# Kernel tuning notes

Measured on AMD Instinct MI355X. Metric: run time of the kernel, lower is better.

Reference implementation:

```python
import jax, jax.numpy as jnp
import numpy as np

N = 50000
E = 800000
D_IN, D_HID, D_OUT = 256, 512, 256
LN_EPS = 1e-5


def setup_inputs() -> dict:
    key = jax.random.key(0)
    ks = jax.random.split(key, 8)
    return {
        "v": jax.random.normal(ks[0], (N, D_IN), dtype=jnp.float32),
        "edge_weight": jax.random.uniform(ks[1], (E,), dtype=jnp.float32),
        "epsilon": jnp.zeros((1, 1), dtype=jnp.float32),
        "w1": jax.random.normal(ks[2], (D_HID, D_IN), dtype=jnp.float32) * (1.0 / np.sqrt(D_IN)),
        "b1": jnp.zeros((D_HID,), dtype=jnp.float32),
        "g1": jnp.ones((D_HID,), dtype=jnp.float32),
        "beta1": jnp.zeros((D_HID,), dtype=jnp.float32),
        "w2": jax.random.normal(ks[3], (D_OUT, D_HID), dtype=jnp.float32) * (1.0 / np.sqrt(D_HID)),
        "b2": jnp.zeros((D_OUT,), dtype=jnp.float32),
        "g2": jnp.ones((D_OUT,), dtype=jnp.float32),
        "beta2": jnp.zeros((D_OUT,), dtype=jnp.float32),
        "src": jax.random.randint(ks[4], (E,), 0, N, dtype=jnp.int32),
        "dst": jax.random.randint(ks[5], (E,), 0, N, dtype=jnp.int32),
    }


def _layer_norm(x, g, b):
    mu = jnp.mean(x, axis=-1, keepdims=True)
    var = jnp.mean(jnp.square(x - mu), axis=-1, keepdims=True)
    return (x - mu) * jax.lax.rsqrt(var + LN_EPS) * g + b


def reference(v, edge_weight, epsilon, w1, b1, g1, beta1, w2, b2, g2, beta2, src, dst):
    # sparse adjacency aggregation: agg[dst] += w * v[src]   (torch.sparse.mm(a, v))
    msgs = v[src] * edge_weight[:, None]            # [E, D_IN]
    agg = jax.ops.segment_sum(msgs, dst, num_segments=v.shape[0])  # [N, D_IN]
    h = agg + epsilon * v                            # epsilon residual
    # MLP: Linear -> LayerNorm -> ReLU  (x2)
    h = jax.nn.relu(_layer_norm(h @ w1.T + b1, g1, beta1))
    h = jax.nn.relu(_layer_norm(h @ w2.T + b2, g2, beta2))
    return h
```

## Files before the change

kernel.cpp:

```cpp
#include <hip/hip_runtime.h>

#define D_IN 256
#define D_HID 512
#define D_OUT 256
#define LN_EPS 1e-5f
#define SCAN_B 512

typedef __attribute__((ext_vector_type(8))) short bf16x8;
typedef __attribute__((ext_vector_type(4))) float f32x4;

__device__ __forceinline__ ushort f2bf(float x) {
    union { float f; unsigned u; } c; c.f = x;
    unsigned r = c.u + 0x7FFFu + ((c.u >> 16) & 1u);
    return (ushort)(r >> 16);
}
__device__ __forceinline__ float bf2f(unsigned b) {
    union { unsigned u; float f; } c; c.u = b << 16;
    return c.f;
}

__global__ void prep_kernel(const float* __restrict__ v, const float* __restrict__ w1,
                            const float* __restrict__ w2, ushort* __restrict__ vb,
                            ushort* __restrict__ w1b, ushort* __restrict__ w2b,
                            int* __restrict__ cnt, int n4v, int nzero,
                            int bv, int bw) {
    int b = blockIdx.x, t = threadIdx.x;
    if (b < bv) {
        int i = b * 256 + t;
        if (i < n4v) {
            float4 x = ((const float4*)v)[i];
            ((ushort4*)vb)[i] = make_ushort4(f2bf(x.x), f2bf(x.y), f2bf(x.z), f2bf(x.w));
        }
    } else if (b < bv + bw) {
        int j = (b - bv) * 256 + t;
        if (j < 32768) {
            float4 x = ((const float4*)w1)[j];
            ((ushort4*)w1b)[j] = make_ushort4(f2bf(x.x), f2bf(x.y), f2bf(x.z), f2bf(x.w));
        } else {
            int k = j - 32768;
            float4 x = ((const float4*)w2)[k];
            ((ushort4*)w2b)[k] = make_ushort4(f2bf(x.x), f2bf(x.y), f2bf(x.z), f2bf(x.w));
        }
    } else {
        int i = (b - bv - bw) * 256 + t;
        if (i < nzero) cnt[i] = 0;
    }
}

__global__ void hist_kernel(const int* __restrict__ dst, int* __restrict__ cnt, int E) {
    int e = blockIdx.x * 256 + threadIdx.x;
    if (e < E) atomicAdd(&cnt[dst[e]], 1);
}

__global__ __launch_bounds__(SCAN_B) void scan1_kernel(const int* __restrict__ cnt,
                                                       int* __restrict__ offs,
                                                       int* __restrict__ bsum, int n) {
    __shared__ int s[SCAN_B];
    int i = blockIdx.x * SCAN_B + threadIdx.x;
    int x = (i < n) ? cnt[i] : 0;
    s[threadIdx.x] = x;
    __syncthreads();
    for (int o = 1; o < SCAN_B; o <<= 1) {
        int t = (threadIdx.x >= (unsigned)o) ? s[threadIdx.x - o] : 0;
        __syncthreads();
        s[threadIdx.x] += t;
        __syncthreads();
    }
    if (i < n) offs[i] = s[threadIdx.x] - x;
    if (threadIdx.x == SCAN_B - 1) bsum[blockIdx.x] = s[threadIdx.x];
}

__global__ __launch_bounds__(SCAN_B) void scan3_kernel(int* __restrict__ offs,
                                                       int* __restrict__ cursor,
                                                       const int* __restrict__ bsum,
                                                       int n, int E, int nb) {
    __shared__ int s[SCAN_B];
    int t = threadIdx.x;
    s[t] = (t < nb && t < (int)blockIdx.x) ? bsum[t] : 0;
    __syncthreads();
    for (int o = SCAN_B / 2; o > 0; o >>= 1) {
        if (t < o) s[t] += s[t + o];
        __syncthreads();
    }
    int base = s[0];
    int i = blockIdx.x * SCAN_B + t;
    if (i < n) {
        int v0 = offs[i] + base;
        offs[i] = v0;
        cursor[i] = v0;
    }
    if (i == 0) offs[n] = E;
}

__global__ void fill_kernel(const int* __restrict__ src, const int* __restrict__ dst,
                            const float* __restrict__ ew, int* __restrict__ cursor,
                            int2* __restrict__ perm, int E) {
    int e = blockIdx.x * 256 + threadIdx.x;
    if (e >= E) return;
    int p = atomicAdd(&cursor[dst[e]], 1);
    perm[p] = make_int2(src[e], __float_as_int(ew[e]));
}

__global__ __launch_bounds__(256) void aggregate_kernel(
    const ushort* __restrict__ vb, const float* __restrict__ eps_p,
    const int* __restrict__ offs, const int2* __restrict__ perm,
    ushort* __restrict__ aggb, int N) {
    int node = blockIdx.x * 4 + (threadIdx.x >> 6);
    if (node >= N) return;
    int lane = threadIdx.x & 63;
    int beg = offs[node], end = offs[node + 1];
    float a0 = 0.f, a1 = 0.f, a2 = 0.f, a3 = 0.f;
    float c0 = 0.f, c1 = 0.f, c2 = 0.f, c3 = 0.f;

    int i = beg;
    for (; i + 8 <= end; i += 8) {
        int2 p0 = perm[i + 0], p1 = perm[i + 1], p2 = perm[i + 2], p3 = perm[i + 3];
        int2 p4 = perm[i + 4], p5 = perm[i + 5], p6 = perm[i + 6], p7 = perm[i + 7];
        float w0 = __int_as_float(p0.y), w1 = __int_as_float(p1.y);
        float w2 = __int_as_float(p2.y), w3 = __int_as_float(p3.y);
        float w4 = __int_as_float(p4.y), w5 = __int_as_float(p5.y);
        float w6 = __int_as_float(p6.y), w7 = __int_as_float(p7.y);
        ushort4 r0 = ((const ushort4*)(vb + (size_t)p0.x * D_IN))[lane];
        ushort4 r1 = ((const ushort4*)(vb + (size_t)p1.x * D_IN))[lane];
        ushort4 r2 = ((const ushort4*)(vb + (size_t)p2.x * D_IN))[lane];
        ushort4 r3 = ((const ushort4*)(vb + (size_t)p3.x * D_IN))[lane];
        ushort4 r4 = ((const ushort4*)(vb + (size_t)p4.x * D_IN))[lane];
        ushort4 r5 = ((const ushort4*)(vb + (size_t)p5.x * D_IN))[lane];
        ushort4 r6 = ((const ushort4*)(vb + (size_t)p6.x * D_IN))[lane];
        ushort4 r7 = ((const ushort4*)(vb + (size_t)p7.x * D_IN))[lane];
        a0 += w0 * bf2f(r0.x) + w1 * bf2f(r1.x) + w2 * bf2f(r2.x) + w3 * bf2f(r3.x);
        a1 += w0 * bf2f(r0.y) + w1 * bf2f(r1.y) + w2 * bf2f(r2.y) + w3 * bf2f(r3.y);
        a2 += w0 * bf2f(r0.z) + w1 * bf2f(r1.z) + w2 * bf2f(r2.z) + w3 * bf2f(r3.z);
        a3 += w0 * bf2f(r0.w) + w1 * bf2f(r1.w) + w2 * bf2f(r2.w) + w3 * bf2f(r3.w);
        c0 += w4 * bf2f(r4.x) + w5 * bf2f(r5.x) + w6 * bf2f(r6.x) + w7 * bf2f(r7.x);
        c1 += w4 * bf2f(r4.y) + w5 * bf2f(r5.y) + w6 * bf2f(r6.y) + w7 * bf2f(r7.y);
        c2 += w4 * bf2f(r4.z) + w5 * bf2f(r5.z) + w6 * bf2f(r6.z) + w7 * bf2f(r7.z);
        c3 += w4 * bf2f(r4.w) + w5 * bf2f(r5.w) + w6 * bf2f(r6.w) + w7 * bf2f(r7.w);
    }
    for (; i + 4 <= end; i += 4) {
        int2 p0 = perm[i + 0], p1 = perm[i + 1], p2 = perm[i + 2], p3 = perm[i + 3];
        float w0 = __int_as_float(p0.y), w1 = __int_as_float(p1.y);
        float w2 = __int_as_float(p2.y), w3 = __int_as_float(p3.y);
        ushort4 r0 = ((const ushort4*)(vb + (size_t)p0.x * D_IN))[lane];
        ushort4 r1 = ((const ushort4*)(vb + (size_t)p1.x * D_IN))[lane];
        ushort4 r2 = ((const ushort4*)(vb + (size_t)p2.x * D_IN))[lane];
        ushort4 r3 = ((const ushort4*)(vb + (size_t)p3.x * D_IN))[lane];
        a0 += w0 * bf2f(r0.x) + w1 * bf2f(r1.x) + w2 * bf2f(r2.x) + w3 * bf2f(r3.x);
        a1 += w0 * bf2f(r0.y) + w1 * bf2f(r1.y) + w2 * bf2f(r2.y) + w3 * bf2f(r3.y);
        a2 += w0 * bf2f(r0.z) + w1 * bf2f(r1.z) + w2 * bf2f(r2.z) + w3 * bf2f(r3.z);
        a3 += w0 * bf2f(r0.w) + w1 * bf2f(r1.w) + w2 * bf2f(r2.w) + w3 * bf2f(r3.w);
    }
    for (; i < end; ++i) {
        int2 p = perm[i];
        float w = __int_as_float(p.y);
        ushort4 r = ((const ushort4*)(vb + (size_t)p.x * D_IN))[lane];
        a0 += w * bf2f(r.x); a1 += w * bf2f(r.y);
        a2 += w * bf2f(r.z); a3 += w * bf2f(r.w);
    }
    a0 += c0; a1 += c1; a2 += c2; a3 += c3;
    float eps = eps_p[0];
    ushort4 m = ((const ushort4*)(vb + (size_t)node * D_IN))[lane];
    a0 += eps * bf2f(m.x); a1 += eps * bf2f(m.y);
    a2 += eps * bf2f(m.z); a3 += eps * bf2f(m.w);
    ((ushort4*)(aggb + (size_t)node * D_IN))[lane] =
        make_ushort4(f2bf(a0), f2bf(a1), f2bf(a2), f2bf(a3));
}

#define HSTR 520
#define BS1_OFF 1024
#define BS2_OFF 16640

__global__ __launch_bounds__(256) void mlp_kernel(
    const ushort* __restrict__ A, const ushort* __restrict__ w1b,
    const ushort* __restrict__ w2b,
    const float* __restrict__ b1, const float* __restrict__ g1, const float* __restrict__ be1,
    const float* __restrict__ b2, const float* __restrict__ g2, const float* __restrict__ be2,
    float* __restrict__ out, int N) {
    __shared__ ushort lds[24832];
    __shared__ float red[2][32][4];
    __shared__ float mu_s[32], rs_s[32];

    int t = threadIdx.x;
    int w = t >> 6, lane = t & 63;
    int row0 = blockIdx.x * 32;
    int fr = lane & 15, q = lane >> 4, kb = q * 8;
    int lrow = lane >> 2, lcol = (lane & 3) * 8;

    f32x4 acc[2][8];
    #pragma unroll
    for (int i = 0; i < 2; ++i)
        #pragma unroll
        for (int c = 0; c < 8; ++c) {
            f32x4 z = {0.f, 0.f, 0.f, 0.f};
            acc[i][c] = z;
        }

    for (int k0 = 0; k0 < D_IN; k0 += 32) {
        if (w < 2) {
            int ar = row0 + w * 16 + lrow;
            if (ar > N - 1) ar = N - 1;
            const ushort* gp = A + (size_t)ar * D_IN + k0 + lcol;
            __builtin_amdgcn_global_load_lds(
                (const __attribute__((address_space(1))) void*)gp,
                (__attribute__((address_space(3))) void*)(&lds[(w * 16) * 32]),
                16, 0, 0);
        }
        #pragma unroll
        for (int c = 0; c < 8; ++c) {
            int br = w * 128 + c * 16 + lrow;
            const ushort* gp = w1b + (size_t)br * D_IN + k0 + lcol;
            __builtin_amdgcn_global_load_lds(
                (const __attribute__((address_space(1))) void*)gp,
                (__attribute__((address_space(3))) void*)(&lds[BS1_OFF + (w * 128 + c * 16) * 32]),
                16, 0, 0);
        }
        __syncthreads();

        bf16x8 af[2], bf[8];
        af[0] = *(const bf16x8*)&lds[fr * 32 + kb];
        af[1] = *(const bf16x8*)&lds[(16 + fr) * 32 + kb];
        #pragma unroll
        for (int c = 0; c < 8; ++c)
            bf[c] = *(const bf16x8*)&lds[BS1_OFF + (w * 128 + c * 16 + fr) * 32 + kb];
        #pragma unroll
        for (int i = 0; i < 2; ++i)
            #pragma unroll
            for (int c = 0; c < 8; ++c)
                acc[i][c] = __builtin_amdgcn_mfma_f32_16x16x32_bf16(af[i], bf[c], acc[i][c], 0, 0, 0);
        __syncthreads();
    }

    {
        float bi[8], gg[8], bb[8];
        #pragma unroll
        for (int c = 0; c < 8; ++c) {
            int col = w * 128 + c * 16 + fr;
            bi[c] = b1[col]; gg[c] = g1[col]; bb[c] = be1[col];
        }
        #pragma unroll
        for (int i = 0; i < 2; ++i) {
            #pragma unroll
            for (int r = 0; r < 4; ++r) {
                float s = 0.f, sq = 0.f;
                #pragma unroll
                for (int c = 0; c < 8; ++c) {
                    float x = acc[i][c][r] + bi[c];
                    acc[i][c][r] = x;
                    s += x; sq += x * x;
                }
                #pragma unroll
                for (int o = 1; o < 16; o <<= 1) {
                    s  += __shfl_xor(s, o, 64);
                    sq += __shfl_xor(sq, o, 64);
                }
                if (fr == 0) {
                    int row = i * 16 + q * 4 + r;
                    red[0][row][w] = s;
                    red[1][row][w] = sq;
                }
            }
        }
        __syncthreads();
        if (t < 32) {
            float s  = red[0][t][0] + red[0][t][1] + red[0][t][2] + red[0][t][3];
            float sq = red[1][t][0] + red[1][t][1] + red[1][t][2] + red[1][t][3];
            float mu = s / (float)D_HID;
            float var = sq / (float)D_HID - mu * mu;
            mu_s[t] = mu;
            rs_s[t] = rsqrtf(var + LN_EPS);
        }
        __syncthreads();
        #pragma unroll
        for (int i = 0; i < 2; ++i) {
            #pragma unroll
            for (int r = 0; r < 4; ++r) {
                int row = i * 16 + q * 4 + r;
                float mu = mu_s[row], rs = rs_s[row];
                #pragma unroll
                for (int c = 0; c < 8; ++c) {
                    int col = w * 128 + c * 16 + fr;
                    float y = (acc[i][c][r] - mu) * rs * gg[c] + bb[c];
                    lds[row * HSTR + col] = f2bf(fmaxf(y, 0.f));
                }
            }
        }
    }

    f32x4 acc2[2][4];
    #pragma unroll
    for (int i = 0; i < 2; ++i)
        #pragma unroll
        for (int c = 0; c < 4; ++c) {
            f32x4 z = {0.f, 0.f, 0.f, 0.f};
            acc2[i][c] = z;
        }

    for (int k0 = 0; k0 < D_HID; k0 += 32) {
        #pragma unroll
        for (int c = 0; c < 4; ++c) {
            int br = w * 64 + c * 16 + lrow;
            const ushort* gp = w2b + (size_t)br * D_HID + k0 + lcol;
            __builtin_amdgcn_global_load_lds(
                (const __attribute__((address_space(1))) void*)gp,
                (__attribute__((address_space(3))) void*)(&lds[BS2_OFF + (w * 64 + c * 16) * 32]),
                16, 0, 0);
        }
        __syncthreads();

        bf16x8 af[2], bf[4];
        af[0] = *(const bf16x8*)&lds[fr * HSTR + k0 + kb];
        af[1] = *(const bf16x8*)&lds[(16 + fr) * HSTR + k0 + kb];
        #pragma unroll
        for (int c = 0; c < 4; ++c)
            bf[c] = *(const bf16x8*)&lds[BS2_OFF + (w * 64 + c * 16 + fr) * 32 + kb];
        #pragma unroll
        for (int i = 0; i < 2; ++i)
            #pragma unroll
            for (int c = 0; c < 4; ++c)
                acc2[i][c] = __builtin_amdgcn_mfma_f32_16x16x32_bf16(af[i], bf[c], acc2[i][c], 0, 0, 0);
        __syncthreads();
    }

    {
        float bi[4], gg[4], bb[4];
        #pragma unroll
        for (int c = 0; c < 4; ++c) {
            int col = w * 64 + c * 16 + fr;
            bi[c] = b2[col]; gg[c] = g2[col]; bb[c] = be2[col];
        }
        #pragma unroll
        for (int i = 0; i < 2; ++i) {
            #pragma unroll
            for (int r = 0; r < 4; ++r) {
                float s = 0.f, sq = 0.f;
                #pragma unroll
                for (int c = 0; c < 4; ++c) {
                    float x = acc2[i][c][r] + bi[c];
                    acc2[i][c][r] = x;
                    s += x; sq += x * x;
                }
                #pragma unroll
                for (int o = 1; o < 16; o <<= 1) {
                    s  += __shfl_xor(s, o, 64);
                    sq += __shfl_xor(sq, o, 64);
                }
                if (fr == 0) {
                    int row = i * 16 + q * 4 + r;
                    red[0][row][w] = s;
                    red[1][row][w] = sq;
                }
            }
        }
        __syncthreads();
        if (t < 32) {
            float s  = red[0][t][0] + red[0][t][1] + red[0][t][2] + red[0][t][3];
            float sq = red[1][t][0] + red[1][t][1] + red[1][t][2] + red[1][t][3];
            float mu = s / (float)D_OUT;
            float var = sq / (float)D_OUT - mu * mu;
            mu_s[t] = mu;
            rs_s[t] = rsqrtf(var + LN_EPS);
        }
        __syncthreads();
        #pragma unroll
        for (int i = 0; i < 2; ++i) {
            #pragma unroll
            for (int r = 0; r < 4; ++r) {
                int row = i * 16 + q * 4 + r;
                int grow = row0 + row;
                if (grow >= N) continue;
                float mu = mu_s[row], rs = rs_s[row];
                #pragma unroll
                for (int c = 0; c < 4; ++c) {
                    int col = w * 64 + c * 16 + fr;
                    float y = (acc2[i][c][r] - mu) * rs * gg[c] + bb[c];
                    out[(size_t)grow * D_OUT + col] = fmaxf(y, 0.f);
                }
            }
        }
    }
}

extern "C" void kernel_launch(void* const* d_in, const int* in_sizes, int n_in,
                              void* d_out, int out_size, void* d_ws, size_t ws_size,
                              hipStream_t stream) {
    const float* v     = (const float*)d_in[0];
    const float* ew    = (const float*)d_in[1];
    const float* eps   = (const float*)d_in[2];
    const float* w1    = (const float*)d_in[3];
    const float* b1    = (const float*)d_in[4];
    const float* g1    = (const float*)d_in[5];
    const float* beta1 = (const float*)d_in[6];
    const float* w2    = (const float*)d_in[7];
    const float* b2    = (const float*)d_in[8];
    const float* g2    = (const float*)d_in[9];
    const float* beta2 = (const float*)d_in[10];
    const int*   src   = (const int*)d_in[11];
    const int*   dst   = (const int*)d_in[12];

    int N = in_sizes[0] / D_IN;
    int E = in_sizes[1];

    float* out = (float*)d_out;

    char* ws = (char*)d_ws;
    size_t off = 0;
    ushort* vb   = (ushort*)(ws + off); off += (size_t)N * D_IN * 2;
    ushort* aggb = (ushort*)(ws + off); off += (size_t)N * D_IN * 2;
    ushort* w1b  = (ushort*)(ws + off); off += (size_t)D_HID * D_IN * 2;
    ushort* w2b  = (ushort*)(ws + off); off += (size_t)D_OUT * D_HID * 2;
    int* offs     = (int*)(ws + off); off += (size_t)(N + 256) * 4;
    int* cursor   = (int*)(ws + off); off += (size_t)(N + 256) * 4;
    int* bsum     = (int*)(ws + off); off += 1024;
    int2* perm    = (int2*)(ws + off); off += (size_t)E * 8;

    int nb = (N + SCAN_B - 1) / SCAN_B;
    int n4v = N * (D_IN / 4);
    int bv = (n4v + 255) / 256;
    int bw = 256;
    int bz = (N + 255) / 256;

    prep_kernel<<<bv + bw + bz, 256, 0, stream>>>(v, w1, w2, vb, w1b, w2b,
                                                  cursor, n4v, N, bv, bw);

    hist_kernel<<<(E + 255) / 256, 256, 0, stream>>>(dst, cursor, E);
    scan1_kernel<<<nb, SCAN_B, 0, stream>>>(cursor, offs, bsum, N);
    scan3_kernel<<<nb, SCAN_B, 0, stream>>>(offs, cursor, bsum, N, E, nb);
    fill_kernel<<<(E + 255) / 256, 256, 0, stream>>>(src, dst, ew, cursor, perm, E);

    aggregate_kernel<<<(N + 3) / 4, 256, 0, stream>>>(vb, eps, offs, perm, aggb, N);

    int mblocks = (N + 31) / 32;
    mlp_kernel<<<mblocks, 256, 0, stream>>>(aggb, w1b, w2b,
                                            b1, g1, beta1, b2, g2, beta2, out, N);
}
```

Measured before the change: 358.2 us.

## Double MLP row tile to 64 and swizzle hidden-activation LDS layout

The fused MLP kernel now processes 64 rows per block instead of 32, so each weight tile loaded into LDS is reused across twice as many MFMA row fragments, halving weight traffic per row. The hidden activation buffer drops the padded stride in favour of an XOR swizzle to avoid bank conflicts, and the LayerNorm reduction scratch is aliased into the weight-2 staging region. This raises register use (accumulators double) and LDS to about 80KB per block, with launch bounds requesting two blocks per CU, which may limit occupancy or cause spills.

```diff
diff --git a/kernel.cpp b/kernel.cpp
--- a/kernel.cpp
+++ b/kernel.cpp
@@ -166,37 +166,36 @@
         make_ushort4(f2bf(a0), f2bf(a1), f2bf(a2), f2bf(a3));
 }
 
-#define HSTR 520
-#define BS1_OFF 1024
-#define BS2_OFF 16640
-
-__global__ __launch_bounds__(256) void mlp_kernel(
+#define BS1_OFF 2048
+#define BS2_OFF 32768
+#define HS_IDX(row, col) ((row) * 512 + ((col) ^ (((row) & 7) << 3)))
+
+__global__ __launch_bounds__(256, 2) void mlp_kernel(
     const ushort* __restrict__ A, const ushort* __restrict__ w1b,
     const ushort* __restrict__ w2b,
     const float* __restrict__ b1, const float* __restrict__ g1, const float* __restrict__ be1,
     const float* __restrict__ b2, const float* __restrict__ g2, const float* __restrict__ be2,
     float* __restrict__ out, int N) {
-    __shared__ ushort lds[24832];
-    __shared__ float red[2][32][4];
-    __shared__ float mu_s[32], rs_s[32];
+    __shared__ ushort lds[40960];
+    float* redf = (float*)&lds[BS2_OFF];
 
     int t = threadIdx.x;
     int w = t >> 6, lane = t & 63;
-    int row0 = blockIdx.x * 32;
+    int row0 = blockIdx.x * 64;
     int fr = lane & 15, q = lane >> 4, kb = q * 8;
     int lrow = lane >> 2, lcol = (lane & 3) * 8;
 
-    f32x4 acc[2][8];
+    f32x4 acc[4][8];
     #pragma unroll
-    for (int i = 0; i < 2; ++i)
+    for (int m = 0; m < 4; ++m)
         #pragma unroll
         for (int c = 0; c < 8; ++c) {
             f32x4 z = {0.f, 0.f, 0.f, 0.f};
-            acc[i][c] = z;
+            acc[m][c] = z;
         }
 
     for (int k0 = 0; k0 < D_IN; k0 += 32) {
-        if (w < 2) {
+        {
             int ar = row0 + w * 16 + lrow;
             if (ar > N - 1) ar = N - 1;
             const ushort* gp = A + (size_t)ar * D_IN + k0 + lcol;
@@ -216,17 +215,18 @@
         }
         __syncthreads();
 
-        bf16x8 af[2], bf[8];
-        af[0] = *(const bf16x8*)&lds[fr * 32 + kb];
-        af[1] = *(const bf16x8*)&lds[(16 + fr) * 32 + kb];
+        bf16x8 af[4], bf[8];
+        #pragma unroll
+        for (int m = 0; m < 4; ++m)
+            af[m] = *(const bf16x8*)&lds[(m * 16 + fr) * 32 + kb];
         #pragma unroll
         for (int c = 0; c < 8; ++c)
             bf[c] = *(const bf16x8*)&lds[BS1_OFF + (w * 128 + c * 16 + fr) * 32 + kb];
         #pragma unroll
-        for (int i = 0; i < 2; ++i)
+        for (int m = 0; m < 4; ++m)
             #pragma unroll
             for (int c = 0; c < 8; ++c)
-                acc[i][c] = __builtin_amdgcn_mfma_f32_16x16x32_bf16(af[i], bf[c], acc[i][c], 0, 0, 0);
+                acc[m][c] = __builtin_amdgcn_mfma_f32_16x16x32_bf16(af[m], bf[c], acc[m][c], 0, 0, 0);
         __syncthreads();
     }
 
@@ -238,14 +238,14 @@
             bi[c] = b1[col]; gg[c] = g1[col]; bb[c] = be1[col];
         }
         #pragma unroll
-        for (int i = 0; i < 2; ++i) {
+        for (int m = 0; m < 4; ++m) {
             #pragma unroll
             for (int r = 0; r < 4; ++r) {
                 float s = 0.f, sq = 0.f;
                 #pragma unroll
                 for (int c = 0; c < 8; ++c) {
-                    float x = acc[i][c][r] + bi[c];
-                    acc[i][c][r] = x;
+                    float x = acc[m][c][r] + bi[c];
+                    acc[m][c][r] = x;
                     s += x; sq += x * x;
                 }
                 #pragma unroll
@@ -254,45 +254,47 @@
                     sq += __shfl_xor(sq, o, 64);
                 }
                 if (fr == 0) {
-                    int row = i * 16 + q * 4 + r;
-                    red[0][row][w] = s;
-                    red[1][row][w] = sq;
+                    int row = m * 16 + q * 4 + r;
+                    redf[row * 4 + w]       = s;
+                    redf[256 + row * 4 + w] = sq;
                 }
             }
         }
         __syncthreads();
-        if (t < 32) {
-            float s  = red[0][t][0] + red[0][t][1] + red[0][t][2] + red[0][t][3];
-            float sq = red[1][t][0] + red[1][t][1] + red[1][t][2] + red[1][t][3];
+        if (t < 64) {
+            float s  = redf[t * 4 + 0] + redf[t * 4 + 1] + redf[t * 4 + 2] + redf[t * 4 + 3];
+            float sq = redf[256 + t * 4 + 0] + redf[256 + t * 4 + 1] +
+                       redf[256 + t * 4 + 2] + redf[256 + t * 4 + 3];
             float mu = s / (float)D_HID;
             float var = sq / (float)D_HID - mu * mu;
-            mu_s[t] = mu;
-            rs_s[t] = rsqrtf(var + LN_EPS);
-        }
-        __syncthreads();
-        #pragma unroll
-        for (int i = 0; i < 2; ++i) {
+            redf[512 + t] = mu;
+            redf[576 + t] = rsqrtf(var + LN_EPS);
+        }
+        __syncthreads();
+        #pragma unroll
+        for (int m = 0; m < 4; ++m) {
             #pragma unroll
             for (int r = 0; r < 4; ++r) {
-                int row = i * 16 + q * 4 + r;
-                float mu = mu_s[row], rs = rs_s[row];
+                int row = m * 16 + q * 4 + r;
+                float mu = redf[512 + row], rs = redf[576 + row];
                 #pragma unroll
                 for (int c = 0; c < 8; ++c) {
                     int col = w * 128 + c * 16 + fr;
-                    float y = (acc[i][c][r] - mu) * rs * gg[c] + bb[c];
-                    lds[row * HSTR + col] = f2bf(fmaxf(y, 0.f));
+                    float y = (acc[m][c][r] - mu) * rs * gg[c] + bb[c];
+                    lds[HS_IDX(row, col)] = f2bf(fmaxf(y, 0.f));
                 }
             }
         }
     }
-
-    f32x4 acc2[2][4];
+    __syncthreads();
+
+    f32x4 acc2[4][4];
     #pragma unroll
-    for (int i = 0; i < 2; ++i)
+    for (int m = 0; m < 4; ++m)
         #pragma unroll
         for (int c = 0; c < 4; ++c) {
             f32x4 z = {0.f, 0.f, 0.f, 0.f};
-            acc2[i][c] = z;
+            acc2[m][c] = z;
         }
 
     for (int k0 = 0; k0 < D_HID; k0 += 32) {
@@ -307,17 +309,20 @@
         }
         __syncthreads();
 
-        bf16x8 af[2], bf[4];
-        af[0] = *(const bf16x8*)&lds[fr * HSTR + k0 + kb];
-        af[1] = *(const bf16x8*)&lds[(16 + fr) * HSTR + k0 + kb];
+        bf16x8 af[4], bf[4];
+        #pragma unroll
+        for (int m = 0; m < 4; ++m) {
+            int row = m * 16 + fr;
+            af[m] = *(const bf16x8*)&lds[HS_IDX(row, k0 + kb)];
+        }
         #pragma unroll
         for (int c = 0; c < 4; ++c)
             bf[c] = *(const bf16x8*)&lds[BS2_OFF + (w * 64 + c * 16 + fr) * 32 + kb];
         #pragma unroll
-        for (int i = 0; i < 2; ++i)
+        for (int m = 0; m < 4; ++m)
             #pragma unroll
             for (int c = 0; c < 4; ++c)
-                acc2[i][c] = __builtin_amdgcn_mfma_f32_16x16x32_bf16(af[i], bf[c], acc2[i][c], 0, 0, 0);
+                acc2[m][c] = __builtin_amdgcn_mfma_f32_16x16x32_bf16(af[m], bf[c], acc2[m][c], 0, 0, 0);
         __syncthreads();
     }
 
@@ -329,14 +334,14 @@
             bi[c] = b2[col]; gg[c] = g2[col]; bb[c] = be2[col];
         }
         #pragma unroll
-        for (int i = 0; i < 2; ++i) {
+        for (int m = 0; m < 4; ++m) {
             #pragma unroll
             for (int r = 0; r < 4; ++r) {
                 float s = 0.f, sq = 0.f;
                 #pragma unroll
                 for (int c = 0; c < 4; ++c) {
-                    float x = acc2[i][c][r] + bi[c];
-                    acc2[i][c][r] = x;
+                    float x = acc2[m][c][r] + bi[c];
+                    acc2[m][c][r] = x;
                     s += x; sq += x * x;
                 }
                 #pragma unroll
@@ -345,34 +350,35 @@
                     sq += __shfl_xor(sq, o, 64);
                 }
                 if (fr == 0) {
-                    int row = i * 16 + q * 4 + r;
-                    red[0][row][w] = s;
-                    red[1][row][w] = sq;
+                    int row = m * 16 + q * 4 + r;
+                    redf[row * 4 + w]       = s;
+                    redf[256 + row * 4 + w] = sq;
                 }
             }
         }
         __syncthreads();
-        if (t < 32) {
-            float s  = red[0][t][0] + red[0][t][1] + red[0][t][2] + red[0][t][3];
-            float sq = red[1][t][0] + red[1][t][1] + red[1][t][2] + red[1][t][3];
+        if (t < 64) {
+            float s  = redf[t * 4 + 0] + redf[t * 4 + 1] + redf[t * 4 + 2] + redf[t * 4 + 3];
+            float sq = redf[256 + t * 4 + 0] + redf[256 + t * 4 + 1] +
+                       redf[256 + t * 4 + 2] + redf[256 + t * 4 + 3];
             float mu = s / (float)D_OUT;
             float var = sq / (float)D_OUT - mu * mu;
-            mu_s[t] = mu;
-            rs_s[t] = rsqrtf(var + LN_EPS);
-        }
-        __syncthreads();
-        #pragma unroll
-        for (int i = 0; i < 2; ++i) {
+            redf[512 + t] = mu;
+            redf[576 + t] = rsqrtf(var + LN_EPS);
+        }
+        __syncthreads();
+        #pragma unroll
+        for (int m = 0; m < 4; ++m) {
             #pragma unroll
             for (int r = 0; r < 4; ++r) {
-                int row = i * 16 + q * 4 + r;
+                int row = m * 16 + q * 4 + r;
                 int grow = row0 + row;
                 if (grow >= N) continue;
-                float mu = mu_s[row], rs = rs_s[row];
+                float mu = redf[512 + row], rs = redf[576 + row];
                 #pragma unroll
                 for (int c = 0; c < 4; ++c) {
                     int col = w * 64 + c * 16 + fr;
-                    float y = (acc2[i][c][r] - mu) * rs * gg[c] + bb[c];
+                    float y = (acc2[m][c][r] - mu) * rs * gg[c] + bb[c];
                     out[(size_t)grow * D_OUT + col] = fmaxf(y, 0.f);
                 }
             }
@@ -429,7 +435,7 @@
 
     aggregate_kernel<<<(N + 3) / 4, 256, 0, stream>>>(vb, eps, offs, perm, aggb, N);
 
-    int mblocks = (N + 31) / 32;
+    int mblocks = (N + 63) / 64;
     mlp_kernel<<<mblocks, 256, 0, stream>>>(aggb, w1b, w2b,
                                             b1, g1, beta1, b2, g2, beta2, out, N);
 }
```

Result: faster. 332.4 us (-7.2%).
